# Kernel optimization log

Measured on AMD Instinct MI355X. Metric: run time of the kernel, lower is better.

## Reference

```python
import jax, jax.numpy as jnp
import numpy as np

BN_EPS = 1e-5

def _bn(x, p):
    # p rows: gamma, beta, running_mean, running_var (eval-mode BatchNorm1d)
    g, b, m, v = p[0], p[1], p[2], p[3]
    return (x - m) * jax.lax.rsqrt(v + BN_EPS) * g + b

def setup_inputs() -> dict:
    key = jax.random.key(0)
    ks = iter(jax.random.split(key, 32))
    B, P, T, E, H = 16, 64, 8, 64, 64
    batch = B * P
    def w(shape, scale=0.1):
        return (jax.random.normal(next(ks), shape, dtype=jnp.float32) * scale)
    def bn_pack(d):
        k1, k2, k3, k4 = jax.random.split(next(ks), 4)
        gamma = 1.0 + 0.1 * jax.random.normal(k1, (d,), dtype=jnp.float32)
        beta = 0.1 * jax.random.normal(k2, (d,), dtype=jnp.float32)
        mean = 0.1 * jax.random.normal(k3, (d,), dtype=jnp.float32)
        var = 0.5 + jax.random.uniform(k4, (d,), dtype=jnp.float32)
        return jnp.stack([gamma, beta, mean, var], axis=0)
    return {
        "h_states": w((1, batch, H), 1.0),
        "end_pos": w((batch, 2), 1.0),
        "vx": w((T, batch), 1.0),
        "vy": w((T, batch), 1.0),
        "agent_type": jax.random.uniform(next(ks), (T, batch, 1), dtype=jnp.float32),
        "ws_w": w((2, E)), "ws_b": w((E,)),
        "wv_w": w((2, E)), "wv_b": w((E,)),
        "wa_w": w((6, E)), "wa_b": w((E,)),
        "att1_w": w((E, 1024)), "att1_b": w((1024,)), "att_bn1": bn_pack(1024),
        "att2_w": w((1024, 1)), "att2_b": w((1,)), "att_bn2": bn_pack(1),
        "pre1_w": w((E + H, 512)), "pre1_b": w((512,)), "pre_bn1": bn_pack(512),
        "pre2_w": w((512, 1024)), "pre2_b": w((1024,)), "pre_bn2": bn_pack(1024),
        "num_ped": P,
    }

def reference(h_states, end_pos, vx, vy, agent_type,
              ws_w, ws_b, wv_w, wv_b, wa_w, wa_b,
              att1_w, att1_b, att_bn1, att2_w, att2_b, att_bn2,
              pre1_w, pre1_b, pre_bn1, pre2_w, pre2_b, pre_bn2,
              num_ped):
    P = num_ped
    batch = end_pos.shape[0]
    B = batch // P  # uniform groups (seq_start_end = [(b*P, (b+1)*P)])
    H = h_states.shape[-1]
    h = h_states.reshape(batch, H).reshape(B, P, H)            # curr_hidden per group
    pos = end_pos.reshape(B, P, 2)
    # k = i*P + j: repeated row = pos[j], 'transposed' row = pos[i]
    rel = pos[:, None, :, :] - pos[:, :, None, :]               # [B, i, j, 2]
    rel_emb = rel @ ws_w + ws_b                                 # [B, i, j, E]
    # attention_mlp: Linear->BN->ReLU->Linear->BN->ReLU (make_mlp applies BN+act after every layer)
    a1 = jax.nn.relu(_bn(rel_emb @ att1_w + att1_b, att_bn1))   # [B, i, j, 1024]
    scores = jax.nn.relu(_bn(a1 @ att2_w + att2_b, att_bn2))    # [B, i, j, 1]
    # torch.softmax(scores, dim=1) on shape (n*n, 1): softmax over a singleton -> all ones
    aw = jax.nn.softmax(scores, axis=-1)
    # velocity embedding: computed in the original then discarded (dead code, kept for fidelity)
    vel = jnp.stack([vx[-1].reshape(B, P), vy[-1].reshape(B, P)], axis=-1)
    _vel_emb = vel @ wv_w + wv_b  # noqa: F841 (unused, matches original)
    # curr_agent_type.repeat(num_ped, 6): row k=i*P+j -> type[j] tiled to 6 features
    at6 = jnp.repeat(agent_type[0].reshape(B, P, 1), 6, axis=-1)  # [B, j, 6]
    at_emb = at6 @ wa_w + wa_b                                    # [B, j, E]
    feat_j = jnp.concatenate([h, at_emb], axis=-1)                # [B, j, H+E]
    weighted = jnp.broadcast_to(feat_j[:, None, :, :], (B, P, P, feat_j.shape[-1])) * (0.05 * aw)
    p1 = jax.nn.relu(_bn(weighted @ pre1_w + pre1_b, pre_bn1))    # [B, i, j, 512]
    p2 = jax.nn.relu(_bn(p1 @ pre2_w + pre2_b, pre_bn2))          # [B, i, j, 1024]
    pool = p2.max(axis=2)                                         # view(n,n,-1).max(1): max over j
    return pool.reshape(batch, -1)
```

## Files before the change

kernel.cpp:

```cpp
#include <hip/hip_runtime.h>
#include <hip/hip_bf16.h>

#define BN_EPS 1e-5f

typedef float f32x4 __attribute__((ext_vector_type(4)));
typedef __bf16 bfx8 __attribute__((ext_vector_type(8)));
typedef __bf16 bfx4 __attribute__((ext_vector_type(4)));


__global__ __launch_bounds__(256) void k0_prep(
    const float* __restrict__ w2, const float* __restrict__ w1,
    const float* __restrict__ h, const float* __restrict__ at,
    const float* __restrict__ wa_w, const float* __restrict__ wa_b,
    const float* __restrict__ b1, const float* __restrict__ bn1,
    const float* __restrict__ b2, const float* __restrict__ bn2,
    __bf16* __restrict__ w2t, __bf16* __restrict__ w1t,
    __bf16* __restrict__ xg, float* __restrict__ scsh)
{
    const int t  = threadIdx.x;
    const int bx = blockIdx.x;

    if (bx < 136) {
        __shared__ float tile[64][69];
        int kt0, n0, src_ld, dst_ld;
        const float* src;
        __bf16* dst;
        if (bx < 128) {
            kt0 = (bx & 7) * 64;  n0 = (bx >> 3) * 64;
            src = w2; src_ld = 1024; dst = w2t; dst_ld = 512;
        } else {
            kt0 = 0;  n0 = (bx - 128) * 64;
            src = w1; src_ld = 512; dst = w1t; dst_ld = 64;
        }
        #pragma unroll
        for (int i = 0; i < 4; ++i) {
            const int idx = t + i * 256;
            const int kk  = idx >> 4;
            const int nq  = (idx & 15) * 4;
            const f32x4 val = *(const f32x4*)&src[(size_t)(kt0 + kk) * src_ld + n0 + nq];
            #pragma unroll
            for (int j = 0; j < 4; ++j) tile[kk][nq + j] = val[j];
        }
        __syncthreads();
        #pragma unroll
        for (int i = 0; i < 2; ++i) {
            const int idx = t + i * 256;
            const int n   = idx >> 3;
            const int kq  = (idx & 7) * 8;
            bfx8 o;
            #pragma unroll
            for (int j = 0; j < 8; ++j) o[j] = (__bf16)tile[kq + j][n];
            *(bfx8*)&dst[(size_t)(n0 + n) * dst_ld + kt0 + kq] = o;
        }
    } else if (bx < 152) {
        const int r0 = (bx - 136) * 64;
        #pragma unroll
        for (int i = 0; i < 2; ++i) {
            const int idx = t + i * 256;
            const int row = idx >> 3;
            const int cg  = (idx & 7) * 8;
            const f32x4 v0 = *(const f32x4*)&h[(size_t)(r0 + row) * 64 + cg];
            const f32x4 v1 = *(const f32x4*)&h[(size_t)(r0 + row) * 64 + cg + 4];
            bfx8 o;
            #pragma unroll
            for (int j = 0; j < 4; ++j) {
                o[j]     = (__bf16)(0.05f * v0[j]);
                o[4 + j] = (__bf16)(0.05f * v1[j]);
            }
            *(bfx8*)&xg[(size_t)(r0 + row) * 64 + cg] = o;
        }
    } else if (bx < 160) {
        __shared__ float Sl[64], Wbl[64];
        __shared__ float pu[4][64], pv[4][64];
        const int c0 = (bx - 152) * 64;
        if (t < 64) {
            float s = 0.f;
            #pragma unroll
            for (int q = 0; q < 6; ++q) s += wa_w[q * 64 + t];
            Sl[t]  = 0.05f * s;
            Wbl[t] = 0.05f * wa_b[t];
        }
        __syncthreads();
        const int cl   = t & 63;
        const int eseg = t >> 6;
        float su = 0.f, sv = 0.f;
        for (int e = eseg * 16; e < eseg * 16 + 16; ++e) {
            const float w = w1[(size_t)(64 + e) * 512 + c0 + cl];
            su = fmaf(Sl[e], w, su);
            sv = fmaf(Wbl[e], w, sv);
        }
        pu[eseg][cl] = su;
        pv[eseg][cl] = sv;
        __syncthreads();
        if (t < 64) {
            const int c = c0 + t;
            const float u = pu[0][t] + pu[1][t] + pu[2][t] + pu[3][t];
            const float v = pv[0][t] + pv[1][t] + pv[2][t] + pv[3][t];
            const float s = rsqrtf(bn1[1536 + c] + BN_EPS) * bn1[c];
            const float base = (b1[c] - bn1[1024 + c]) * s + bn1[512 + c];
            scsh[c]        = s;
            scsh[512 + c]  = u * s;
            scsh[1024 + c] = v * s + base;
        }
    } else {
        #pragma unroll
        for (int i = 0; i < 4; ++i) {
            const int c = t + i * 256;
            const float s  = rsqrtf(bn2[3072 + c] + BN_EPS) * bn2[c];
            scsh[1536 + c] = s;
            scsh[2560 + c] = (b2[c] - bn2[2048 + c]) * s + bn2[1024 + c];
        }
    }
}

__global__ __launch_bounds__(512, 2) void kmain(
    const __bf16* __restrict__ xg,
    const __bf16* __restrict__ w1t,
    const __bf16* __restrict__ w2t,
    const float* __restrict__ at,
    const float* __restrict__ scsh,
    float* __restrict__ out)
{
    const int cc   = blockIdx.x;
    const int b    = blockIdx.y;
    const int t    = threadIdx.x;
    const int wid  = t >> 6;
    const int lane = t & 63;
    const int l15  = lane & 15;
    const int lhi  = lane >> 4;
    const int c0w  = wid * 64;

    __shared__ __bf16 x_lds[64][72];
    __shared__ __bf16 p1_lds[64][520];
    __shared__ __bf16 B2_lds[64][520];
    __shared__ float  red[4][64];

    bfx8 xfrag;
    {
        const int row = t >> 3;
        const int cg  = (t & 7) * 8;
        xfrag = *(const bfx8*)&xg[(size_t)(b * 64 + row) * 64 + cg];
    }
    bfx8 b1r[8];
    #pragma unroll
    for (int ks = 0; ks < 2; ++ks)
        #pragma unroll
        for (int cf = 0; cf < 4; ++cf)
            b1r[ks * 4 + cf] = *(const bfx8*)&w1t[
                (size_t)(c0w + cf * 16 + l15) * 64 + ks * 32 + lhi * 8];
    {
        const int row = t >> 3;
        const int cg  = (t & 7) * 8;
        *(bfx8*)&x_lds[row][cg] = xfrag;
    }
    __syncthreads();

    f32x4 b2stage[8];
    {
        const __bf16* base = w2t + (size_t)(cc * 64) * 512;
        #pragma unroll
        for (int i = 0; i < 8; ++i) {
            const int n = i * 8 + wid;
            b2stage[i] = *(const f32x4*)(base + (size_t)n * 512 + lane * 8);
        }
    }
    float at4[4];
    #pragma unroll
    for (int mf = 0; mf < 4; ++mf) at4[mf] = at[b * 64 + mf * 16 + l15];
    f32x4 sc[4], us[4], vs[4];
    #pragma unroll
    for (int cf = 0; cf < 4; ++cf) {
        const int c4 = c0w + cf * 16 + lhi * 4;
        sc[cf] = *(const f32x4*)&scsh[c4];
        us[cf] = *(const f32x4*)&scsh[512 + c4];
        vs[cf] = *(const f32x4*)&scsh[1024 + c4];
    }

    f32x4 acc1[4][4] = {};
    #pragma unroll
    for (int ks = 0; ks < 2; ++ks) {
        bfx8 bf_[4];
        #pragma unroll
        for (int mf = 0; mf < 4; ++mf)
            bf_[mf] = *(const bfx8*)&x_lds[mf * 16 + l15][ks * 32 + lhi * 8];
        #pragma unroll
        for (int cf = 0; cf < 4; ++cf)
            #pragma unroll
            for (int mf = 0; mf < 4; ++mf)
                acc1[cf][mf] = __builtin_amdgcn_mfma_f32_16x16x32_bf16(
                    b1r[ks * 4 + cf], bf_[mf], acc1[cf][mf], 0, 0, 0);
    }

    #pragma unroll
    for (int i = 0; i < 8; ++i) {
        const int n = i * 8 + wid;
        *(f32x4*)((char*)&B2_lds[0][0] + (size_t)n * 1040 + lane * 16) =
            b2stage[i];
    }
    #pragma unroll
    for (int cf = 0; cf < 4; ++cf)
        #pragma unroll
        for (int mf = 0; mf < 4; ++mf) {
            bfx4 pk;
            #pragma unroll
            for (int r = 0; r < 4; ++r) {
                const float base = fmaf(at4[mf], us[cf][r], vs[cf][r]);
                pk[r] = (__bf16)fmaxf(
                    fmaf(acc1[cf][mf][r], sc[cf][r], base), 0.f);
            }
            *(bfx4*)&p1_lds[mf * 16 + l15][c0w + cf * 16 + lhi * 4] = pk;
        }
    __syncthreads();

    const int mrow  = (wid >> 1) * 16;
    const int nbase = (wid & 1) * 32;
    float s2[2], h2[2];
    #pragma unroll
    for (int nf = 0; nf < 2; ++nf) {
        const int ng = cc * 64 + nbase + nf * 16 + l15;
        s2[nf] = scsh[1536 + ng];
        h2[nf] = scsh[2560 + ng];
    }
    f32x4 acc2[2] = {};
    #pragma unroll
    for (int ks = 0; ks < 16; ++ks) {
        const bfx8 a = *(const bfx8*)&p1_lds[mrow + l15][ks * 32 + lhi * 8];
        #pragma unroll
        for (int nf = 0; nf < 2; ++nf) {
            const bfx8 bb =
                *(const bfx8*)&B2_lds[nbase + nf * 16 + l15][ks * 32 + lhi * 8];
            acc2[nf] = __builtin_amdgcn_mfma_f32_16x16x32_bf16(a, bb, acc2[nf], 0, 0, 0);
        }
    }

    #pragma unroll
    for (int nf = 0; nf < 2; ++nf) {
        float mm = 0.f;
        #pragma unroll
        for (int r = 0; r < 4; ++r)
            mm = fmaxf(mm, fmaxf(fmaf(acc2[nf][r], s2[nf], h2[nf]), 0.f));
        mm = fmaxf(mm, __shfl_xor(mm, 16));
        mm = fmaxf(mm, __shfl_xor(mm, 32));
        if (lane < 16) red[wid >> 1][nbase + nf * 16 + lane] = mm;
    }
    __syncthreads();

    #pragma unroll
    for (int i = 0; i < 2; ++i) {
        const int q   = t + i * 512;
        const int row = q >> 4;
        const int cq  = (q & 15) * 4;
        const f32x4 r0 = *(const f32x4*)&red[0][cq];
        const f32x4 r1 = *(const f32x4*)&red[1][cq];
        const f32x4 r2 = *(const f32x4*)&red[2][cq];
        const f32x4 r3 = *(const f32x4*)&red[3][cq];
        f32x4 pv;
        #pragma unroll
        for (int j = 0; j < 4; ++j)
            pv[j] = fmaxf(fmaxf(r0[j], r1[j]), fmaxf(r2[j], r3[j]));
        *(f32x4*)&out[(size_t)(b * 64 + row) * 1024 + cc * 64 + cq] = pv;
    }
}

extern "C" void kernel_launch(void* const* d_in, const int* in_sizes, int n_in,
                              void* d_out, int out_size, void* d_ws, size_t ws_size,
                              hipStream_t stream) {
    const float* h    = (const float*)d_in[0];
    const float* at   = (const float*)d_in[4];
    const float* wa_w = (const float*)d_in[9];
    const float* wa_b = (const float*)d_in[10];
    const float* w1   = (const float*)d_in[17];
    const float* b1   = (const float*)d_in[18];
    const float* bn1  = (const float*)d_in[19];
    const float* w2   = (const float*)d_in[20];
    const float* b2   = (const float*)d_in[21];
    const float* bn2  = (const float*)d_in[22];

    char* ws = (char*)d_ws;
    __bf16* w2t  = (__bf16*)ws;
    __bf16* w1t  = (__bf16*)(ws + (1 << 20));
    __bf16* xg   = (__bf16*)(ws + (1 << 20) + (64 << 10));
    float*  scsh = (float*)(ws + (1 << 20) + (192 << 10));
    float*  out  = (float*)d_out;

    k0_prep<<<161, 256, 0, stream>>>(w2, w1, h, at, wa_w, wa_b,
                                     b1, bn1, b2, bn2, w2t, w1t, xg, scsh);
    kmain<<<dim3(16, 16), 512, 0, stream>>>(xg, w1t, w2t, at, scsh, out);
}
```

Baseline: 17.59 us.

## Stream W2 directly into LDS and retile second GEMM onto four waves

The W2 tile now goes straight from global memory to LDS with global_load_lds, replacing the register staging and the later LDS store. The x fragments are read from global memory directly into MFMA operand registers, which removes x_lds and one block barrier. The second GEMM runs on only four waves, each computing a 2x2 fragment tile so more MFMAs share each LDS operand read. The cost is that half the waves sit idle during that GEMM, and the async LDS fill relies on correct wait handling before the barrier.

```diff
diff --git a/kernel.cpp b/kernel.cpp
--- a/kernel.cpp
+++ b/kernel.cpp
@@ -6,6 +6,9 @@
 typedef float f32x4 __attribute__((ext_vector_type(4)));
 typedef __bf16 bfx8 __attribute__((ext_vector_type(8)));
 typedef __bf16 bfx4 __attribute__((ext_vector_type(4)));
+
+#define GBL_AS(p) ((const __attribute__((address_space(1))) void*)(p))
+#define LDS_AS(p) ((__attribute__((address_space(3))) void*)(p))
 
 
 __global__ __launch_bounds__(256) void k0_prep(
@@ -130,17 +133,18 @@
     const int lhi  = lane >> 4;
     const int c0w  = wid * 64;
 
-    __shared__ __bf16 x_lds[64][72];
     __shared__ __bf16 p1_lds[64][520];
     __shared__ __bf16 B2_lds[64][520];
-    __shared__ float  red[4][64];
-
-    bfx8 xfrag;
-    {
-        const int row = t >> 3;
-        const int cg  = (t & 7) * 8;
-        xfrag = *(const bfx8*)&xg[(size_t)(b * 64 + row) * 64 + cg];
-    }
+    __shared__ float  red[2][64];
+
+    bfx8 xfr[2][4];
+    #pragma unroll
+    for (int ks = 0; ks < 2; ++ks)
+        #pragma unroll
+        for (int mf = 0; mf < 4; ++mf)
+            xfr[ks][mf] = *(const bfx8*)&xg[
+                (size_t)(b * 64 + mf * 16 + l15) * 64 + ks * 32 + lhi * 8];
+
     bfx8 b1r[8];
     #pragma unroll
     for (int ks = 0; ks < 2; ++ks)
@@ -148,22 +152,7 @@
         for (int cf = 0; cf < 4; ++cf)
             b1r[ks * 4 + cf] = *(const bfx8*)&w1t[
                 (size_t)(c0w + cf * 16 + l15) * 64 + ks * 32 + lhi * 8];
-    {
-        const int row = t >> 3;
-        const int cg  = (t & 7) * 8;
-        *(bfx8*)&x_lds[row][cg] = xfrag;
-    }
-    __syncthreads();
-
-    f32x4 b2stage[8];
-    {
-        const __bf16* base = w2t + (size_t)(cc * 64) * 512;
-        #pragma unroll
-        for (int i = 0; i < 8; ++i) {
-            const int n = i * 8 + wid;
-            b2stage[i] = *(const f32x4*)(base + (size_t)n * 512 + lane * 8);
-        }
-    }
+
     float at4[4];
     #pragma unroll
     for (int mf = 0; mf < 4; ++mf) at4[mf] = at[b * 64 + mf * 16 + l15];
@@ -175,28 +164,35 @@
         us[cf] = *(const f32x4*)&scsh[512 + c4];
         vs[cf] = *(const f32x4*)&scsh[1024 + c4];
     }
+    const int w  = wid & 3;
+    const int mw = w >> 1;
+    const int nw = w & 1;
+    float s2[2], h2[2];
+    #pragma unroll
+    for (int nf = 0; nf < 2; ++nf) {
+        const int ng = cc * 64 + nw * 32 + nf * 16 + l15;
+        s2[nf] = scsh[1536 + ng];
+        h2[nf] = scsh[2560 + ng];
+    }
+
+    #pragma unroll
+    for (int i = 0; i < 8; ++i) {
+        const int n = i * 8 + wid;
+        __builtin_amdgcn_global_load_lds(
+            GBL_AS(w2t + (size_t)(cc * 64 + n) * 512 + lane * 8),
+            LDS_AS(&B2_lds[n][0]), 16, 0, 0);
+    }
 
     f32x4 acc1[4][4] = {};
     #pragma unroll
-    for (int ks = 0; ks < 2; ++ks) {
-        bfx8 bf_[4];
-        #pragma unroll
-        for (int mf = 0; mf < 4; ++mf)
-            bf_[mf] = *(const bfx8*)&x_lds[mf * 16 + l15][ks * 32 + lhi * 8];
+    for (int ks = 0; ks < 2; ++ks)
         #pragma unroll
         for (int cf = 0; cf < 4; ++cf)
             #pragma unroll
             for (int mf = 0; mf < 4; ++mf)
                 acc1[cf][mf] = __builtin_amdgcn_mfma_f32_16x16x32_bf16(
-                    b1r[ks * 4 + cf], bf_[mf], acc1[cf][mf], 0, 0, 0);
-    }
-
-    #pragma unroll
-    for (int i = 0; i < 8; ++i) {
-        const int n = i * 8 + wid;
-        *(f32x4*)((char*)&B2_lds[0][0] + (size_t)n * 1040 + lane * 16) =
-            b2stage[i];
-    }
+                    b1r[ks * 4 + cf], xfr[ks][mf], acc1[cf][mf], 0, 0, 0);
+
     #pragma unroll
     for (int cf = 0; cf < 4; ++cf)
         #pragma unroll
@@ -212,36 +208,39 @@
         }
     __syncthreads();
 
-    const int mrow  = (wid >> 1) * 16;
-    const int nbase = (wid & 1) * 32;
-    float s2[2], h2[2];
-    #pragma unroll
-    for (int nf = 0; nf < 2; ++nf) {
-        const int ng = cc * 64 + nbase + nf * 16 + l15;
-        s2[nf] = scsh[1536 + ng];
-        h2[nf] = scsh[2560 + ng];
-    }
-    f32x4 acc2[2] = {};
-    #pragma unroll
-    for (int ks = 0; ks < 16; ++ks) {
-        const bfx8 a = *(const bfx8*)&p1_lds[mrow + l15][ks * 32 + lhi * 8];
+    if (wid < 4) {
+        f32x4 acc2[2][2] = {};
+        #pragma unroll
+        for (int ks = 0; ks < 16; ++ks) {
+            bfx8 a[2], bb[2];
+            #pragma unroll
+            for (int mf = 0; mf < 2; ++mf)
+                a[mf] = *(const bfx8*)&p1_lds[mw * 32 + mf * 16 + l15]
+                                             [ks * 32 + lhi * 8];
+            #pragma unroll
+            for (int nf = 0; nf < 2; ++nf)
+                bb[nf] = *(const bfx8*)&B2_lds[nw * 32 + nf * 16 + l15]
+                                              [ks * 32 + lhi * 8];
+            #pragma unroll
+            for (int mf = 0; mf < 2; ++mf)
+                #pragma unroll
+                for (int nf = 0; nf < 2; ++nf)
+                    acc2[mf][nf] = __builtin_amdgcn_mfma_f32_16x16x32_bf16(
+                        a[mf], bb[nf], acc2[mf][nf], 0, 0, 0);
+        }
         #pragma unroll
         for (int nf = 0; nf < 2; ++nf) {
-            const bfx8 bb =
-                *(const bfx8*)&B2_lds[nbase + nf * 16 + l15][ks * 32 + lhi * 8];
-            acc2[nf] = __builtin_amdgcn_mfma_f32_16x16x32_bf16(a, bb, acc2[nf], 0, 0, 0);
-        }
-    }
-
-    #pragma unroll
-    for (int nf = 0; nf < 2; ++nf) {
-        float mm = 0.f;
-        #pragma unroll
-        for (int r = 0; r < 4; ++r)
-            mm = fmaxf(mm, fmaxf(fmaf(acc2[nf][r], s2[nf], h2[nf]), 0.f));
-        mm = fmaxf(mm, __shfl_xor(mm, 16));
-        mm = fmaxf(mm, __shfl_xor(mm, 32));
-        if (lane < 16) red[wid >> 1][nbase + nf * 16 + lane] = mm;
+            float mm = 0.f;
+            #pragma unroll
+            for (int mf = 0; mf < 2; ++mf)
+                #pragma unroll
+                for (int r = 0; r < 4; ++r)
+                    mm = fmaxf(mm, fmaxf(
+                        fmaf(acc2[mf][nf][r], s2[nf], h2[nf]), 0.f));
+            mm = fmaxf(mm, __shfl_xor(mm, 16));
+            mm = fmaxf(mm, __shfl_xor(mm, 32));
+            if (lane < 16) red[mw][nw * 32 + nf * 16 + lane] = mm;
+        }
     }
     __syncthreads();
 
@@ -252,12 +251,10 @@
         const int cq  = (q & 15) * 4;
         const f32x4 r0 = *(const f32x4*)&red[0][cq];
         const f32x4 r1 = *(const f32x4*)&red[1][cq];
-        const f32x4 r2 = *(const f32x4*)&red[2][cq];
-        const f32x4 r3 = *(const f32x4*)&red[3][cq];
         f32x4 pv;
         #pragma unroll
         for (int j = 0; j < 4; ++j)
-            pv[j] = fmaxf(fmaxf(r0[j], r1[j]), fmaxf(r2[j], r3[j]));
+            pv[j] = fmaxf(r0[j], r1[j]);
         *(f32x4*)&out[(size_t)(b * 64 + row) * 1024 + cc * 64 + cq] = pv;
     }
 }
```

Measured after the change: 18.69 us. +6.3%, slower.

## Pipeline GEMM1/GEMM2 over K-chunks with double-buffered p1 and halve output tile

Applied to the files above, without the earlier changes.

The main kernel now computes the 512-wide hidden layer in 64-column chunks, double-buffering each chunk in small LDS tiles. GEMM2 on the current chunk is interleaved with GEMM1 on the next, and the weight fragments are prefetched straight into registers two chunks ahead. Each block produces 32 output columns instead of 64, so the grid doubles to 32x16, and the launch bounds request 4 blocks per CU thanks to the much smaller LDS footprint. The aim is more parallelism and occupancy with less LDS staging. The cost is that GEMM1 is recomputed twice as often across blocks, and there are now many more barriers.

```diff
diff --git a/kernel.cpp b/kernel.cpp
--- a/kernel.cpp
+++ b/kernel.cpp
@@ -113,7 +113,7 @@
     }
 }
 
-__global__ __launch_bounds__(512, 2) void kmain(
+__global__ __launch_bounds__(512, 4) void kmain(
     const __bf16* __restrict__ xg,
     const __bf16* __restrict__ w1t,
     const __bf16* __restrict__ w2t,
@@ -128,137 +128,128 @@
     const int lane = t & 63;
     const int l15  = lane & 15;
     const int lhi  = lane >> 4;
-    const int c0w  = wid * 64;
+
+    const int mw = wid >> 1;
+    const int cw = wid & 1;
+    const int nw = wid & 1;
 
     __shared__ __bf16 x_lds[64][72];
-    __shared__ __bf16 p1_lds[64][520];
-    __shared__ __bf16 B2_lds[64][520];
-    __shared__ float  red[4][64];
-
-    bfx8 xfrag;
+    __shared__ __bf16 p1c[2][64][72];
+    __shared__ float  red[4][32];
+
     {
         const int row = t >> 3;
         const int cg  = (t & 7) * 8;
-        xfrag = *(const bfx8*)&xg[(size_t)(b * 64 + row) * 64 + cg];
-    }
-    bfx8 b1r[8];
+        *(bfx8*)&x_lds[row][cg] = *(const bfx8*)&xg[(size_t)(b * 64 + row) * 64 + cg];
+    }
+    const float at1 = at[b * 64 + mw * 16 + l15];
+    const int   ng  = cc * 32 + nw * 16 + l15;
+    const float s2  = scsh[1536 + ng];
+    const float h2  = scsh[2560 + ng];
+
+    bfx8 b1r[2][4];
+    bfx8 b2f[2][2];
+    f32x4 sc[2], us[2], vs[2];
+
+    #define LOAD_B1R(ck, par)                                                 \
+        _Pragma("unroll")                                                     \
+        for (int ks = 0; ks < 2; ++ks)                                        \
+            _Pragma("unroll")                                                 \
+            for (int cf = 0; cf < 2; ++cf)                                    \
+                b1r[par][ks * 2 + cf] = *(const bfx8*)&w1t[                   \
+                    (size_t)((ck) * 64 + cw * 32 + cf * 16 + l15) * 64 +      \
+                    ks * 32 + lhi * 8];
+
+    #define LOAD_B2(ck, par)                                                  \
+        _Pragma("unroll")                                                     \
+        for (int ks = 0; ks < 2; ++ks)                                        \
+            b2f[par][ks] = *(const bfx8*)&w2t[                                \
+                (size_t)(cc * 32 + nw * 16 + l15) * 512 + (ck) * 64 +         \
+                ks * 32 + lhi * 8];
+
+    #define LOAD_PRM(ck)                                                      \
+        _Pragma("unroll")                                                     \
+        for (int cf = 0; cf < 2; ++cf) {                                      \
+            const int c4 = (ck) * 64 + cw * 32 + cf * 16 + lhi * 4;           \
+            sc[cf] = *(const f32x4*)&scsh[c4];                                \
+            us[cf] = *(const f32x4*)&scsh[512 + c4];                          \
+            vs[cf] = *(const f32x4*)&scsh[1024 + c4];                         \
+        }
+
+    #define GEMM1(ck, par, buf)                                               \
+        {                                                                     \
+            bfx8 xf[2];                                                       \
+            _Pragma("unroll")                                                 \
+            for (int ks = 0; ks < 2; ++ks)                                    \
+                xf[ks] = *(const bfx8*)&x_lds[mw * 16 + l15][ks * 32 + lhi * 8]; \
+            f32x4 acc1[2] = {};                                               \
+            _Pragma("unroll")                                                 \
+            for (int ks = 0; ks < 2; ++ks)                                    \
+                _Pragma("unroll")                                             \
+                for (int cf = 0; cf < 2; ++cf)                                \
+                    acc1[cf] = __builtin_amdgcn_mfma_f32_16x16x32_bf16(       \
+                        b1r[par][ks * 2 + cf], xf[ks], acc1[cf], 0, 0, 0);    \
+            _Pragma("unroll")                                                 \
+            for (int cf = 0; cf < 2; ++cf) {                                  \
+                bfx4 pk;                                                      \
+                _Pragma("unroll")                                             \
+                for (int r = 0; r < 4; ++r) {                                 \
+                    const float base = fmaf(at1, us[cf][r], vs[cf][r]);       \
+                    pk[r] = (__bf16)fmaxf(                                    \
+                        fmaf(acc1[cf][r], sc[cf][r], base), 0.f);             \
+                }                                                             \
+                *(bfx4*)&p1c[buf][mw * 16 + l15][cw * 32 + cf * 16 + lhi * 4] = pk; \
+            }                                                                 \
+        }
+
+    LOAD_B1R(0, 0)
+    LOAD_PRM(0)
+    LOAD_B2(0, 0)
+    __syncthreads();
+    GEMM1(0, 0, 0)
+    LOAD_B1R(1, 1)
+    __syncthreads();
+
+    f32x4 acc2 = {};
     #pragma unroll
-    for (int ks = 0; ks < 2; ++ks)
-        #pragma unroll
-        for (int cf = 0; cf < 4; ++cf)
-            b1r[ks * 4 + cf] = *(const bfx8*)&w1t[
-                (size_t)(c0w + cf * 16 + l15) * 64 + ks * 32 + lhi * 8];
+    for (int ck = 0; ck < 8; ++ck) {
+        const int par  = ck & 1;
+        const int npar = par ^ 1;
+        if (ck < 7) { LOAD_B2(ck + 1, npar) LOAD_PRM(ck + 1) }
+        if (ck < 6) { LOAD_B1R(ck + 2, par) }
+        #pragma unroll
+        for (int ks = 0; ks < 2; ++ks) {
+            const bfx8 a = *(const bfx8*)&p1c[par][mw * 16 + l15][ks * 32 + lhi * 8];
+            acc2 = __builtin_amdgcn_mfma_f32_16x16x32_bf16(
+                a, b2f[par][ks], acc2, 0, 0, 0);
+        }
+        if (ck < 7) { GEMM1(ck + 1, npar, npar) }
+        __syncthreads();
+    }
+
+    {
+        float mm = 0.f;
+        #pragma unroll
+        for (int r = 0; r < 4; ++r)
+            mm = fmaxf(mm, fmaxf(fmaf(acc2[r], s2, h2), 0.f));
+        mm = fmaxf(mm, __shfl_xor(mm, 16));
+        mm = fmaxf(mm, __shfl_xor(mm, 32));
+        if (lane < 16) red[mw][nw * 16 + lane] = mm;
+    }
+    __syncthreads();
+
     {
         const int row = t >> 3;
-        const int cg  = (t & 7) * 8;
-        *(bfx8*)&x_lds[row][cg] = xfrag;
-    }
-    __syncthreads();
-
-    f32x4 b2stage[8];
-    {
-        const __bf16* base = w2t + (size_t)(cc * 64) * 512;
-        #pragma unroll
-        for (int i = 0; i < 8; ++i) {
-            const int n = i * 8 + wid;
-            b2stage[i] = *(const f32x4*)(base + (size_t)n * 512 + lane * 8);
-        }
-    }
-    float at4[4];
-    #pragma unroll
-    for (int mf = 0; mf < 4; ++mf) at4[mf] = at[b * 64 + mf * 16 + l15];
-    f32x4 sc[4], us[4], vs[4];
-    #pragma unroll
-    for (int cf = 0; cf < 4; ++cf) {
-        const int c4 = c0w + cf * 16 + lhi * 4;
-        sc[cf] = *(const f32x4*)&scsh[c4];
-        us[cf] = *(const f32x4*)&scsh[512 + c4];
-        vs[cf] = *(const f32x4*)&scsh[1024 + c4];
-    }
-
-    f32x4 acc1[4][4] = {};
-    #pragma unroll
-    for (int ks = 0; ks < 2; ++ks) {
-        bfx8 bf_[4];
-        #pragma unroll
-        for (int mf = 0; mf < 4; ++mf)
-            bf_[mf] = *(const bfx8*)&x_lds[mf * 16 + l15][ks * 32 + lhi * 8];
-        #pragma unroll
-        for (int cf = 0; cf < 4; ++cf)
-            #pragma unroll
-            for (int mf = 0; mf < 4; ++mf)
-                acc1[cf][mf] = __builtin_amdgcn_mfma_f32_16x16x32_bf16(
-                    b1r[ks * 4 + cf], bf_[mf], acc1[cf][mf], 0, 0, 0);
-    }
-
-    #pragma unroll
-    for (int i = 0; i < 8; ++i) {
-        const int n = i * 8 + wid;
-        *(f32x4*)((char*)&B2_lds[0][0] + (size_t)n * 1040 + lane * 16) =
-            b2stage[i];
-    }
-    #pragma unroll
-    for (int cf = 0; cf < 4; ++cf)
-        #pragma unroll
-        for (int mf = 0; mf < 4; ++mf) {
-            bfx4 pk;
-            #pragma unroll
-            for (int r = 0; r < 4; ++r) {
-                const float base = fmaf(at4[mf], us[cf][r], vs[cf][r]);
-                pk[r] = (__bf16)fmaxf(
-                    fmaf(acc1[cf][mf][r], sc[cf][r], base), 0.f);
-            }
-            *(bfx4*)&p1_lds[mf * 16 + l15][c0w + cf * 16 + lhi * 4] = pk;
-        }
-    __syncthreads();
-
-    const int mrow  = (wid >> 1) * 16;
-    const int nbase = (wid & 1) * 32;
-    float s2[2], h2[2];
-    #pragma unroll
-    for (int nf = 0; nf < 2; ++nf) {
-        const int ng = cc * 64 + nbase + nf * 16 + l15;
-        s2[nf] = scsh[1536 + ng];
-        h2[nf] = scsh[2560 + ng];
-    }
-    f32x4 acc2[2] = {};
-    #pragma unroll
-    for (int ks = 0; ks < 16; ++ks) {
-        const bfx8 a = *(const bfx8*)&p1_lds[mrow + l15][ks * 32 + lhi * 8];
-        #pragma unroll
-        for (int nf = 0; nf < 2; ++nf) {
-            const bfx8 bb =
-                *(const bfx8*)&B2_lds[nbase + nf * 16 + l15][ks * 32 + lhi * 8];
-            acc2[nf] = __builtin_amdgcn_mfma_f32_16x16x32_bf16(a, bb, acc2[nf], 0, 0, 0);
-        }
-    }
-
-    #pragma unroll
-    for (int nf = 0; nf < 2; ++nf) {
-        float mm = 0.f;
-        #pragma unroll
-        for (int r = 0; r < 4; ++r)
-            mm = fmaxf(mm, fmaxf(fmaf(acc2[nf][r], s2[nf], h2[nf]), 0.f));
-        mm = fmaxf(mm, __shfl_xor(mm, 16));
-        mm = fmaxf(mm, __shfl_xor(mm, 32));
-        if (lane < 16) red[wid >> 1][nbase + nf * 16 + lane] = mm;
-    }
-    __syncthreads();
-
-    #pragma unroll
-    for (int i = 0; i < 2; ++i) {
-        const int q   = t + i * 512;
-        const int row = q >> 4;
-        const int cq  = (q & 15) * 4;
-        const f32x4 r0 = *(const f32x4*)&red[0][cq];
-        const f32x4 r1 = *(const f32x4*)&red[1][cq];
-        const f32x4 r2 = *(const f32x4*)&red[2][cq];
-        const f32x4 r3 = *(const f32x4*)&red[3][cq];
+        const int cg  = (t & 7) * 4;
+        const f32x4 r0 = *(const f32x4*)&red[0][cg];
+        const f32x4 r1 = *(const f32x4*)&red[1][cg];
+        const f32x4 r2 = *(const f32x4*)&red[2][cg];
+        const f32x4 r3 = *(const f32x4*)&red[3][cg];
         f32x4 pv;
         #pragma unroll
         for (int j = 0; j < 4; ++j)
             pv[j] = fmaxf(fmaxf(r0[j], r1[j]), fmaxf(r2[j], r3[j]));
-        *(f32x4*)&out[(size_t)(b * 64 + row) * 1024 + cc * 64 + cq] = pv;
+        *(f32x4*)&out[(size_t)(b * 64 + row) * 1024 + cc * 32 + cg] = pv;
     }
 }
 
@@ -285,5 +276,5 @@
 
     k0_prep<<<161, 256, 0, stream>>>(w2, w1, h, at, wa_w, wa_b,
                                      b1, bn1, b2, bn2, w2t, w1t, xg, scsh);
-    kmain<<<dim3(16, 16), 512, 0, stream>>>(xg, w1t, w2t, at, scsh, out);
+    kmain<<<dim3(32, 16), 512, 0, stream>>>(xg, w1t, w2t, at, scsh, out);
 }
```

Result: slower. 38.56 us (+119.2%).
